# Kernel tuning notes

Measured on AMD Instinct MI355X. Metric: run time of the kernel, lower is better.

The kernel has to match this reference:

```python
import jax, jax.numpy as jnp
import numpy as np

N = 50000   # active sparse voxels
B = 4       # batch size
FIN = 64
FOUT = 128
TEMB = 256
K = 27      # 3x3x3 kernel offsets
EPS = 1e-5


def _bn(x, gamma, beta, mean, var):
    # inference-style BatchNorm over channel dim
    return (x - mean) * jax.lax.rsqrt(var + EPS) * gamma + beta


def _sparse_conv(feats, nbr, mask, W):
    # submanifold sparse conv via kernel map:
    # out[n] = sum_k mask[k,n] * feats[nbr[k,n]] @ W[k]
    g = feats[nbr] * mask[..., None].astype(feats.dtype)   # [K, N, Fin]
    return jnp.einsum('knf,kfo->no', g, W)                  # [N, Fout]


def _make_kernel_map(k_nbr, k_msk, n):
    nbr = jax.random.randint(k_nbr, (K, N), 0, n, dtype=jnp.int32)
    mask = jax.random.bernoulli(k_msk, 0.4, (K, N))
    # center offset is the identity map and always valid (submanifold conv)
    nbr = nbr.at[K // 2].set(jnp.arange(N, dtype=jnp.int32))
    mask = mask.at[K // 2].set(True)
    return nbr, mask


def setup_inputs() -> dict:
    key = jax.random.key(0)
    ks = jax.random.split(key, 20)
    x_feats = jax.random.normal(ks[0], (N, FIN), jnp.float32)
    batch_idx = jax.random.randint(ks[1], (N,), 0, B, dtype=jnp.int32)
    t = jax.random.normal(ks[2], (B, TEMB), jnp.float32)
    nbr1, mask1 = _make_kernel_map(ks[3], ks[4], N)
    nbr2, mask2 = _make_kernel_map(ks[5], ks[6], N)
    s1 = 1.0 / np.sqrt(FIN * K)
    s2 = 1.0 / np.sqrt(FOUT * K)
    return {
        'x_feats': x_feats, 'batch_idx': batch_idx, 't': t,
        'nbr1': nbr1, 'mask1': mask1, 'nbr2': nbr2, 'mask2': mask2,
        'bn1_gamma': jnp.ones((FIN,), jnp.float32),
        'bn1_beta': jnp.zeros((FIN,), jnp.float32),
        'bn1_mean': 0.1 * jax.random.normal(ks[7], (FIN,), jnp.float32),
        'bn1_var': jax.random.uniform(ks[8], (FIN,), jnp.float32, 0.5, 1.5),
        'W1': s1 * jax.random.normal(ks[9], (K, FIN, FOUT), jnp.float32),
        't_W': (1.0 / np.sqrt(TEMB)) * jax.random.normal(ks[10], (TEMB, FOUT), jnp.float32),
        't_b': jnp.zeros((FOUT,), jnp.float32),
        'bn2_gamma': jnp.ones((FOUT,), jnp.float32),
        'bn2_beta': jnp.zeros((FOUT,), jnp.float32),
        'bn2_mean': 0.1 * jax.random.normal(ks[11], (FOUT,), jnp.float32),
        'bn2_var': jax.random.uniform(ks[12], (FOUT,), jnp.float32, 0.5, 1.5),
        'W2': s2 * jax.random.normal(ks[13], (K, FOUT, FOUT), jnp.float32),
        'res_W': (1.0 / np.sqrt(FIN)) * jax.random.normal(ks[14], (FIN, FOUT), jnp.float32),
        'res_b': jnp.zeros((FOUT,), jnp.float32),
    }


def reference(x_feats, batch_idx, t, nbr1, mask1, nbr2, mask2,
              bn1_gamma, bn1_beta, bn1_mean, bn1_var, W1,
              t_W, t_b,
              bn2_gamma, bn2_beta, bn2_mean, bn2_var, W2,
              res_W, res_b):
    # conv1 block: BN -> SiLU -> sparse Conv3d
    h = jax.nn.silu(_bn(x_feats, bn1_gamma, bn1_beta, bn1_mean, bn1_var))
    h = _sparse_conv(h, nbr1, mask1, W1)                      # [N, FOUT]
    # FiLM-style time embedding, broadcast per point via batch index
    t_emb = jax.nn.silu(t) @ t_W + t_b                        # [B, FOUT]
    h = h + t_emb[batch_idx]
    # conv2 block
    h2 = jax.nn.silu(_bn(h, bn2_gamma, bn2_beta, bn2_mean, bn2_var))
    h2 = _sparse_conv(h2, nbr2, mask2, W2)                    # [N, FOUT]
    # residual connection (f_in != f_out -> Linear)
    return h2 + (x_feats @ res_W + res_b)
```

## Files before the change

### kernel.cpp

```cpp
#include <hip/hip_runtime.h>


#define EPS 1e-5f

typedef __attribute__((ext_vector_type(8))) short s16x8;
typedef __attribute__((ext_vector_type(4))) float f32x4;
typedef __attribute__((ext_vector_type(4))) unsigned short u16x4;

static __device__ __forceinline__ unsigned short f2bf(float f) {
    union { float f; unsigned u; } v; v.f = f;
    unsigned r = v.u + 0x7fffu + ((v.u >> 16) & 1u);
    return (unsigned short)(r >> 16);
}
static __device__ __forceinline__ float silu_d(float x) {
    return x / (1.f + __expf(-x));
}
static __device__ __forceinline__ void gload_lds16(const void* gsrc, void* ldst) {
    __builtin_amdgcn_global_load_lds(
        (const __attribute__((address_space(1))) unsigned int*)gsrc,
        (__attribute__((address_space(3))) unsigned int*)ldst, 16, 0, 0);
}
static __device__ __forceinline__ int mask_shift(const unsigned char* mask, int NV) {
    size_t base = (size_t)13 * (size_t)NV;
    int v = ((base & 3) == 3) ? 2 : 1;
    return (mask[base + v] == 1) ? 0 : 2;
}

__global__ void k_prep_small(const float* __restrict__ t, const float* __restrict__ tW,
                             const float* __restrict__ tb,
                             const float* __restrict__ g2, const float* __restrict__ b2,
                             const float* __restrict__ m2, const float* __restrict__ v2,
                             float* __restrict__ temb, float* __restrict__ sc,
                             float* __restrict__ sh, int B) {
    int tid = threadIdx.x;
    if (tid < B * 128) {
        int b = tid >> 7, o = tid & 127;
        float s = 0.f;
        for (int e = 0; e < 256; ++e) {
            float tv = t[b * 256 + e];
            s += silu_d(tv) * tW[e * 128 + o];
        }
        temb[tid] = s + tb[o];
    }
    if (tid < 128) {
        float rstd = rsqrtf(v2[tid] + EPS);
        float s1 = g2[tid] * rstd;
        sc[tid] = s1;
        sh[tid] = b2[tid] - m2[tid] * s1;
    }
}

__global__ __launch_bounds__(256) void k_shuffle(
        const float* __restrict__ W1, const float* __restrict__ W2,
        const float* __restrict__ rW,
        unsigned short* __restrict__ W1s, unsigned short* __restrict__ W2s,
        unsigned short* __restrict__ rWs) {
    int tid = blockIdx.x * 256 + threadIdx.x;
    const int n1 = 432 * 512, n2 = 864 * 512, n3 = 16 * 512;
    if (tid < n1) {
        int f = tid >> 9, r = tid & 511, lane = r >> 3, j = r & 7;
        int mt = f & 7, fk = f >> 3, ks = fk & 1, ko = fk >> 1;
        int fin = ks * 32 + (lane >> 4) * 8 + j;
        int fout = mt * 16 + (lane & 15);
        W1s[tid] = f2bf(W1[(ko * 64 + fin) * 128 + fout]);
    } else if (tid < n1 + n2) {
        int e = tid - n1;
        int f = e >> 9, r = e & 511, lane = r >> 3, j = r & 7;
        int mt = f & 7, fk = f >> 3, ks = fk & 3, ko = fk >> 2;
        int fin = ks * 32 + (lane >> 4) * 8 + j;
        int fout = mt * 16 + (lane & 15);
        W2s[e] = f2bf(W2[(ko * 128 + fin) * 128 + fout]);
    } else if (tid < n1 + n2 + n3) {
        int e = tid - n1 - n2;
        int f = e >> 9, r = e & 511, lane = r >> 3, j = r & 7;
        int mt = f & 7, ks = f >> 3;
        int fin = ks * 32 + (lane >> 4) * 8 + j;
        int fout = mt * 16 + (lane & 15);
        rWs[e] = f2bf(rW[fin * 128 + fout]);
    }
}

__global__ __launch_bounds__(256) void k_elem(
        const float* __restrict__ x,
        const float* __restrict__ g1, const float* __restrict__ b1,
        const float* __restrict__ m1, const float* __restrict__ v1,
        unsigned short* __restrict__ h1, int NV) {
    int tid = blockIdx.x * 256 + threadIdx.x;
    if (tid >= NV * 16) return;
    int n = tid >> 4, c = (tid & 15) << 2;
    f32x4 xv = *(const f32x4*)(x + n * 64 + c);
    f32x4 gv = *(const f32x4*)(g1 + c);
    f32x4 bv = *(const f32x4*)(b1 + c);
    f32x4 mv = *(const f32x4*)(m1 + c);
    f32x4 vv = *(const f32x4*)(v1 + c);
    u16x4 ho;
#pragma unroll
    for (int j = 0; j < 4; ++j) {
        float xn = (xv[j] - mv[j]) * rsqrtf(vv[j] + EPS) * gv[j] + bv[j];
        ho[j] = f2bf(silu_d(xn));
    }
    *(u16x4*)(h1 + n * 64 + c) = ho;
}

__global__ __launch_bounds__(512) void k_conv1(
        const unsigned short* __restrict__ h1, const int* __restrict__ nbr,
        const unsigned char* __restrict__ mask, const unsigned short* __restrict__ W1s,
        const float* __restrict__ temb, const int* __restrict__ bidx,
        const float* __restrict__ bn2sc, const float* __restrict__ bn2sh,
        unsigned short* __restrict__ h2in, int NV) {
    __shared__ unsigned short lds0[8192];
    __shared__ unsigned short lds1[8192];
    const int lane = threadIdx.x & 63;
    const int wave = threadIdx.x >> 6;
    const int g = lane >> 4, col = lane & 15;
    const int v = blockIdx.x * 128 + wave * 16 + col;
    const bool vok = v < NV;
    const int msh = mask_shift(mask, NV);

    f32x4 acc[8];
    const f32x4 z4 = {0.f, 0.f, 0.f, 0.f};
#pragma unroll
    for (int m = 0; m < 8; ++m) acc[m] = z4;
    const s16x8 zz = {0, 0, 0, 0, 0, 0, 0, 0};

    auto loadr = [&](int t) -> int {
        if (!vok) return -1;
        int off = t * NV + v;
        int nv = nbr[off];
        bool mm = mask[(size_t)off << msh] != 0;
        return mm ? nv : -1;
    };

    {
        const char* src = (const char*)W1s + (size_t)threadIdx.x * 16;
        char* dst = (char*)lds0 + (size_t)threadIdx.x * 16;
#pragma unroll
        for (int i = 0; i < 2; ++i)
            gload_lds16(src + i * 8192, dst + i * 8192);
    }
    int rA = loadr(0);
    int rN = loadr(1);
    int r0 = rA < 0 ? 0 : rA;
    s16x8 p0 = *(const s16x8*)(h1 + r0 * 64 + 0 * 32 + g * 8);
    s16x8 p1 = *(const s16x8*)(h1 + r0 * 64 + 1 * 32 + g * 8);
    __syncthreads();

    unsigned short* bufc = lds0;
    unsigned short* bufn = lds1;

    for (int t = 0; t < 27; ++t) {
        s16x8 q0, q1;
        int rN2 = -1;
        if (t < 26) {
            const char* src = (const char*)W1s + (size_t)(t + 1) * 16384 + (size_t)threadIdx.x * 16;
            char* dst = (char*)bufn + (size_t)threadIdx.x * 16;
#pragma unroll
            for (int i = 0; i < 2; ++i)
                gload_lds16(src + i * 8192, dst + i * 8192);
            int rn = rN < 0 ? 0 : rN;
            q0 = *(const s16x8*)(h1 + rn * 64 + 0 * 32 + g * 8);
            q1 = *(const s16x8*)(h1 + rn * 64 + 1 * 32 + g * 8);
        }
        if (t < 25) rN2 = loadr(t + 2);
        const bool m = rA >= 0;
        s16x8 b0 = m ? p0 : zz;
        s16x8 b1 = m ? p1 : zz;
        const unsigned short* wp = bufc + lane * 8;
#pragma unroll
        for (int mt = 0; mt < 8; ++mt) {
            s16x8 a = *(const s16x8*)(wp + (0 * 8 + mt) * 512);
            acc[mt] = __builtin_amdgcn_mfma_f32_16x16x32_bf16(a, b0, acc[mt], 0, 0, 0);
        }
#pragma unroll
        for (int mt = 0; mt < 8; ++mt) {
            s16x8 a = *(const s16x8*)(wp + (1 * 8 + mt) * 512);
            acc[mt] = __builtin_amdgcn_mfma_f32_16x16x32_bf16(a, b1, acc[mt], 0, 0, 0);
        }
        if (t < 26) {
            __syncthreads();
            p0 = q0; p1 = q1;
            rA = rN; rN = rN2;
            unsigned short* tmp = bufc; bufc = bufn; bufn = tmp;
        }
    }

    if (vok) {
        int b = bidx[v];
        const float* te = temb + b * 128;
#pragma unroll
        for (int mt = 0; mt < 8; ++mt) {
            int c = mt * 16 + g * 4;
            f32x4 val = acc[mt];
            f32x4 tv = *(const f32x4*)(te + c);
            f32x4 sc = *(const f32x4*)(bn2sc + c);
            f32x4 sh = *(const f32x4*)(bn2sh + c);
            u16x4 o;
#pragma unroll
            for (int j = 0; j < 4; ++j) {
                float zv = (val[j] + tv[j]) * sc[j] + sh[j];
                o[j] = f2bf(silu_d(zv));
            }
            *(u16x4*)(h2in + v * 128 + c) = o;
        }
    }
}

__global__ __launch_bounds__(512) void k_conv2(
        const unsigned short* __restrict__ h2in, const int* __restrict__ nbr,
        const unsigned char* __restrict__ mask, const unsigned short* __restrict__ W2s,
        const float* __restrict__ x, const unsigned short* __restrict__ rWs,
        const float* __restrict__ resb, float* __restrict__ out, int NV) {
    __shared__ unsigned short lds0[16384];
    __shared__ unsigned short lds1[16384];
    const int lane = threadIdx.x & 63;
    const int wave = threadIdx.x >> 6;
    const int g = lane >> 4, col = lane & 15;
    const int v = blockIdx.x * 128 + wave * 16 + col;
    const bool vok = v < NV;
    const int msh = mask_shift(mask, NV);

    f32x4 acc[8];
    const f32x4 z4 = {0.f, 0.f, 0.f, 0.f};
#pragma unroll
    for (int m = 0; m < 8; ++m) acc[m] = z4;
    const s16x8 zz = {0, 0, 0, 0, 0, 0, 0, 0};

    auto loadr = [&](int t) -> int {
        if (!vok) return -1;
        int off = t * NV + v;
        int nv = nbr[off];
        bool mm = mask[(size_t)off << msh] != 0;
        return mm ? nv : -1;
    };

    {
        const char* src = (const char*)W2s + (size_t)threadIdx.x * 16;
        char* dst = (char*)lds0 + (size_t)threadIdx.x * 16;
#pragma unroll
        for (int i = 0; i < 4; ++i)
            gload_lds16(src + i * 8192, dst + i * 8192);
    }
    int rA = loadr(0);
    int rN = loadr(1);
    int r0 = rA < 0 ? 0 : rA;
    s16x8 p0 = *(const s16x8*)(h2in + r0 * 128 + 0 * 32 + g * 8);
    s16x8 p1 = *(const s16x8*)(h2in + r0 * 128 + 1 * 32 + g * 8);
    s16x8 p2 = *(const s16x8*)(h2in + r0 * 128 + 2 * 32 + g * 8);
    s16x8 p3 = *(const s16x8*)(h2in + r0 * 128 + 3 * 32 + g * 8);

    {
        int rv = vok ? v : 0;
#pragma unroll
        for (int ks = 0; ks < 2; ++ks) {
            f32x4 xa = *(const f32x4*)(x + rv * 64 + ks * 32 + g * 8);
            f32x4 xb = *(const f32x4*)(x + rv * 64 + ks * 32 + g * 8 + 4);
            s16x8 b;
#pragma unroll
            for (int j = 0; j < 4; ++j) {
                b[j]     = (short)f2bf(xa[j]);
                b[j + 4] = (short)f2bf(xb[j]);
            }
            const unsigned short* wp = rWs + ks * 4096 + lane * 8;
#pragma unroll
            for (int mt = 0; mt < 8; ++mt) {
                s16x8 a = *(const s16x8*)(wp + mt * 512);
                acc[mt] = __builtin_amdgcn_mfma_f32_16x16x32_bf16(a, b, acc[mt], 0, 0, 0);
            }
        }
    }
    __syncthreads();

    unsigned short* bufc = lds0;
    unsigned short* bufn = lds1;

    for (int t = 0; t < 27; ++t) {
        s16x8 q0, q1, q2, q3;
        int rN2 = -1;
        if (t < 26) {
            const char* src = (const char*)W2s + (size_t)(t + 1) * 32768 + (size_t)threadIdx.x * 16;
            char* dst = (char*)bufn + (size_t)threadIdx.x * 16;
#pragma unroll
            for (int i = 0; i < 4; ++i)
                gload_lds16(src + i * 8192, dst + i * 8192);
            int rn = rN < 0 ? 0 : rN;
            q0 = *(const s16x8*)(h2in + rn * 128 + 0 * 32 + g * 8);
            q1 = *(const s16x8*)(h2in + rn * 128 + 1 * 32 + g * 8);
            q2 = *(const s16x8*)(h2in + rn * 128 + 2 * 32 + g * 8);
            q3 = *(const s16x8*)(h2in + rn * 128 + 3 * 32 + g * 8);
        }
        if (t < 25) rN2 = loadr(t + 2);
        const bool m = rA >= 0;
        s16x8 b0 = m ? p0 : zz;
        s16x8 b1 = m ? p1 : zz;
        s16x8 b2 = m ? p2 : zz;
        s16x8 b3 = m ? p3 : zz;
        const unsigned short* wp = bufc + lane * 8;
#pragma unroll
        for (int mt = 0; mt < 8; ++mt) {
            s16x8 a = *(const s16x8*)(wp + (0 * 8 + mt) * 512);
            acc[mt] = __builtin_amdgcn_mfma_f32_16x16x32_bf16(a, b0, acc[mt], 0, 0, 0);
        }
#pragma unroll
        for (int mt = 0; mt < 8; ++mt) {
            s16x8 a = *(const s16x8*)(wp + (1 * 8 + mt) * 512);
            acc[mt] = __builtin_amdgcn_mfma_f32_16x16x32_bf16(a, b1, acc[mt], 0, 0, 0);
        }
#pragma unroll
        for (int mt = 0; mt < 8; ++mt) {
            s16x8 a = *(const s16x8*)(wp + (2 * 8 + mt) * 512);
            acc[mt] = __builtin_amdgcn_mfma_f32_16x16x32_bf16(a, b2, acc[mt], 0, 0, 0);
        }
#pragma unroll
        for (int mt = 0; mt < 8; ++mt) {
            s16x8 a = *(const s16x8*)(wp + (3 * 8 + mt) * 512);
            acc[mt] = __builtin_amdgcn_mfma_f32_16x16x32_bf16(a, b3, acc[mt], 0, 0, 0);
        }
        if (t < 26) {
            __syncthreads();
            p0 = q0; p1 = q1; p2 = q2; p3 = q3;
            rA = rN; rN = rN2;
            unsigned short* tmp = bufc; bufc = bufn; bufn = tmp;
        }
    }

    if (vok) {
#pragma unroll
        for (int mt = 0; mt < 8; ++mt) {
            int c = mt * 16 + g * 4;
            f32x4 rr = acc[mt] + *(const f32x4*)(resb + c);
            *(f32x4*)(out + v * 128 + c) = rr;
        }
    }
}

extern "C" void kernel_launch(void* const* d_in, const int* in_sizes, int n_in,
                              void* d_out, int out_size, void* d_ws, size_t ws_size,
                              hipStream_t stream) {
    const float* x          = (const float*)d_in[0];
    const int* bidx         = (const int*)d_in[1];
    const float* t          = (const float*)d_in[2];
    const int* nbr1         = (const int*)d_in[3];
    const unsigned char* mask1 = (const unsigned char*)d_in[4];
    const int* nbr2         = (const int*)d_in[5];
    const unsigned char* mask2 = (const unsigned char*)d_in[6];
    const float* bn1g       = (const float*)d_in[7];
    const float* bn1b       = (const float*)d_in[8];
    const float* bn1m       = (const float*)d_in[9];
    const float* bn1v       = (const float*)d_in[10];
    const float* W1         = (const float*)d_in[11];
    const float* tW         = (const float*)d_in[12];
    const float* tb         = (const float*)d_in[13];
    const float* bn2g       = (const float*)d_in[14];
    const float* bn2b       = (const float*)d_in[15];
    const float* bn2m       = (const float*)d_in[16];
    const float* bn2v       = (const float*)d_in[17];
    const float* W2         = (const float*)d_in[18];
    const float* rW         = (const float*)d_in[19];
    const float* resb       = (const float*)d_in[20];

    const int NV = in_sizes[0] / 64;
    const int B  = in_sizes[2] / 256;
    float* out = (float*)d_out;

    char* ws = (char*)d_ws;
    size_t o_W1s = 0;
    size_t o_W2s = o_W1s + (size_t)432 * 1024;
    size_t o_rWs = o_W2s + (size_t)864 * 1024;
    size_t o_te  = o_rWs + (size_t)16 * 1024;
    size_t o_sc  = o_te  + (size_t)B * 128 * 4;
    size_t o_sh  = o_sc  + 512;
    size_t o_h1  = o_sh  + 512;
    size_t o_h2  = o_h1  + (size_t)NV * 64 * 2;

    unsigned short* W1s  = (unsigned short*)(ws + o_W1s);
    unsigned short* W2s  = (unsigned short*)(ws + o_W2s);
    unsigned short* rWs  = (unsigned short*)(ws + o_rWs);
    float* temb  = (float*)(ws + o_te);
    float* bn2sc = (float*)(ws + o_sc);
    float* bn2sh = (float*)(ws + o_sh);
    unsigned short* h1   = (unsigned short*)(ws + o_h1);
    unsigned short* h2in = (unsigned short*)(ws + o_h2);

    k_prep_small<<<1, 512, 0, stream>>>(t, tW, tb, bn2g, bn2b, bn2m, bn2v,
                                        temb, bn2sc, bn2sh, B);
    {
        int total = (432 + 864 + 16) * 512;
        int grid = (total + 255) / 256;
        k_shuffle<<<grid, 256, 0, stream>>>(W1, W2, rW, W1s, W2s, rWs);
    }
    {
        int total = NV * 16;
        int grid = (total + 255) / 256;
        k_elem<<<grid, 256, 0, stream>>>(x, bn1g, bn1b, bn1m, bn1v, h1, NV);
    }
    {
        int grid = (NV + 127) / 128;
        k_conv1<<<grid, 512, 0, stream>>>(h1, nbr1, mask1, W1s, temb, bidx,
                                          bn2sc, bn2sh, h2in, NV);
        k_conv2<<<grid, 512, 0, stream>>>(h2in, nbr2, mask2, W2s, x, rWs,
                                          resb, out, NV);
    }
}
```

Measured before the change: 138.2 us.

## Fuse prep kernels into one launch and resize conv blocks to 98 voxels

Merges the small time-embedding/BN2 prep, weight shuffle and BN1+SiLU elementwise kernels into a single launch dispatched by block index, removing two kernel launches and their serialization gaps. The conv kernels shrink from 512 to 448 threads (7 waves) with 98 voxels per block, giving about 511 blocks so the work spreads more evenly across the GPU's compute units. Each block still streams the full weight tiles into LDS, so per-voxel weight traffic rises, and 14 of the 112 voxel slots per block sit idle.

After: 122.4 us, median of 2. 1.13x faster.

```diff
diff --git a/kernel.cpp b/kernel.cpp
--- a/kernel.cpp
+++ b/kernel.cpp
@@ -6,6 +6,8 @@
 typedef __attribute__((ext_vector_type(8))) short s16x8;
 typedef __attribute__((ext_vector_type(4))) float f32x4;
 typedef __attribute__((ext_vector_type(4))) unsigned short u16x4;
+
+#define VPB 98
 
 static __device__ __forceinline__ unsigned short f2bf(float f) {
     union { float f; unsigned u; } v; v.f = f;
@@ -26,83 +28,91 @@
     return (mask[base + v] == 1) ? 0 : 2;
 }
 
-__global__ void k_prep_small(const float* __restrict__ t, const float* __restrict__ tW,
-                             const float* __restrict__ tb,
-                             const float* __restrict__ g2, const float* __restrict__ b2,
-                             const float* __restrict__ m2, const float* __restrict__ v2,
-                             float* __restrict__ temb, float* __restrict__ sc,
-                             float* __restrict__ sh, int B) {
-    int tid = threadIdx.x;
-    if (tid < B * 128) {
-        int b = tid >> 7, o = tid & 127;
-        float s = 0.f;
-        for (int e = 0; e < 256; ++e) {
-            float tv = t[b * 256 + e];
-            s += silu_d(tv) * tW[e * 128 + o];
-        }
-        temb[tid] = s + tb[o];
-    }
-    if (tid < 128) {
-        float rstd = rsqrtf(v2[tid] + EPS);
-        float s1 = g2[tid] * rstd;
-        sc[tid] = s1;
-        sh[tid] = b2[tid] - m2[tid] * s1;
-    }
-}
-
-__global__ __launch_bounds__(256) void k_shuffle(
+#define NSH 2624
+__global__ __launch_bounds__(256) void k_prep_fused(
+        const float* __restrict__ t, const float* __restrict__ tW,
+        const float* __restrict__ tb,
+        const float* __restrict__ g2, const float* __restrict__ b2,
+        const float* __restrict__ m2, const float* __restrict__ v2,
+        float* __restrict__ temb, float* __restrict__ sc, float* __restrict__ sh,
         const float* __restrict__ W1, const float* __restrict__ W2,
         const float* __restrict__ rW,
         unsigned short* __restrict__ W1s, unsigned short* __restrict__ W2s,
-        unsigned short* __restrict__ rWs) {
-    int tid = blockIdx.x * 256 + threadIdx.x;
-    const int n1 = 432 * 512, n2 = 864 * 512, n3 = 16 * 512;
-    if (tid < n1) {
-        int f = tid >> 9, r = tid & 511, lane = r >> 3, j = r & 7;
-        int mt = f & 7, fk = f >> 3, ks = fk & 1, ko = fk >> 1;
-        int fin = ks * 32 + (lane >> 4) * 8 + j;
-        int fout = mt * 16 + (lane & 15);
-        W1s[tid] = f2bf(W1[(ko * 64 + fin) * 128 + fout]);
-    } else if (tid < n1 + n2) {
-        int e = tid - n1;
-        int f = e >> 9, r = e & 511, lane = r >> 3, j = r & 7;
-        int mt = f & 7, fk = f >> 3, ks = fk & 3, ko = fk >> 2;
-        int fin = ks * 32 + (lane >> 4) * 8 + j;
-        int fout = mt * 16 + (lane & 15);
-        W2s[e] = f2bf(W2[(ko * 128 + fin) * 128 + fout]);
-    } else if (tid < n1 + n2 + n3) {
-        int e = tid - n1 - n2;
-        int f = e >> 9, r = e & 511, lane = r >> 3, j = r & 7;
-        int mt = f & 7, ks = f >> 3;
-        int fin = ks * 32 + (lane >> 4) * 8 + j;
-        int fout = mt * 16 + (lane & 15);
-        rWs[e] = f2bf(rW[fin * 128 + fout]);
-    }
-}
-
-__global__ __launch_bounds__(256) void k_elem(
+        unsigned short* __restrict__ rWs,
         const float* __restrict__ x,
         const float* __restrict__ g1, const float* __restrict__ b1,
         const float* __restrict__ m1, const float* __restrict__ v1,
-        unsigned short* __restrict__ h1, int NV) {
-    int tid = blockIdx.x * 256 + threadIdx.x;
-    if (tid >= NV * 16) return;
-    int n = tid >> 4, c = (tid & 15) << 2;
-    f32x4 xv = *(const f32x4*)(x + n * 64 + c);
-    f32x4 gv = *(const f32x4*)(g1 + c);
-    f32x4 bv = *(const f32x4*)(b1 + c);
-    f32x4 mv = *(const f32x4*)(m1 + c);
-    f32x4 vv = *(const f32x4*)(v1 + c);
-    u16x4 ho;
-#pragma unroll
-    for (int j = 0; j < 4; ++j) {
-        float xn = (xv[j] - mv[j]) * rsqrtf(vv[j] + EPS) * gv[j] + bv[j];
-        ho[j] = f2bf(silu_d(xn));
-    }
-    *(u16x4*)(h1 + n * 64 + c) = ho;
-}
-
-__global__ __launch_bounds__(512) void k_conv1(
+        unsigned short* __restrict__ h1, int NV, int B) {
+    const int bid = blockIdx.x;
+    if (bid < 2) {
+        int idx = bid * 256 + threadIdx.x;
+        if (idx < B * 128) {
+            int b = idx >> 7, o = idx & 127;
+            float s = 0.f;
+            for (int e = 0; e < 256; ++e) {
+                float tv = t[b * 256 + e];
+                s += silu_d(tv) * tW[e * 128 + o];
+            }
+            temb[idx] = s + tb[o];
+        }
+        return;
+    }
+    if (bid == 2) {
+        int tid = threadIdx.x;
+        if (tid < 128) {
+            float rstd = rsqrtf(v2[tid] + EPS);
+            float s1 = g2[tid] * rstd;
+            sc[tid] = s1;
+            sh[tid] = b2[tid] - m2[tid] * s1;
+        }
+        return;
+    }
+    if (bid < 3 + NSH) {
+        int tid = (bid - 3) * 256 + threadIdx.x;
+        const int n1 = 432 * 512, n2 = 864 * 512, n3 = 16 * 512;
+        if (tid < n1) {
+            int f = tid >> 9, r = tid & 511, lane = r >> 3, j = r & 7;
+            int mt = f & 7, fk = f >> 3, ks = fk & 1, ko = fk >> 1;
+            int fin = ks * 32 + (lane >> 4) * 8 + j;
+            int fout = mt * 16 + (lane & 15);
+            W1s[tid] = f2bf(W1[(ko * 64 + fin) * 128 + fout]);
+        } else if (tid < n1 + n2) {
+            int e = tid - n1;
+            int f = e >> 9, r = e & 511, lane = r >> 3, j = r & 7;
+            int mt = f & 7, fk = f >> 3, ks = fk & 3, ko = fk >> 2;
+            int fin = ks * 32 + (lane >> 4) * 8 + j;
+            int fout = mt * 16 + (lane & 15);
+            W2s[e] = f2bf(W2[(ko * 128 + fin) * 128 + fout]);
+        } else if (tid < n1 + n2 + n3) {
+            int e = tid - n1 - n2;
+            int f = e >> 9, r = e & 511, lane = r >> 3, j = r & 7;
+            int mt = f & 7, ks = f >> 3;
+            int fin = ks * 32 + (lane >> 4) * 8 + j;
+            int fout = mt * 16 + (lane & 15);
+            rWs[e] = f2bf(rW[fin * 128 + fout]);
+        }
+        return;
+    }
+    {
+        int tid = (bid - 3 - NSH) * 256 + threadIdx.x;
+        if (tid >= NV * 16) return;
+        int n = tid >> 4, c = (tid & 15) << 2;
+        f32x4 xv = *(const f32x4*)(x + n * 64 + c);
+        f32x4 gv = *(const f32x4*)(g1 + c);
+        f32x4 bv = *(const f32x4*)(b1 + c);
+        f32x4 mv = *(const f32x4*)(m1 + c);
+        f32x4 vv = *(const f32x4*)(v1 + c);
+        u16x4 ho;
+#pragma unroll
+        for (int j = 0; j < 4; ++j) {
+            float xn = (xv[j] - mv[j]) * rsqrtf(vv[j] + EPS) * gv[j] + bv[j];
+            ho[j] = f2bf(silu_d(xn));
+        }
+        *(u16x4*)(h1 + n * 64 + c) = ho;
+    }
+}
+
+__global__ __launch_bounds__(448) void k_conv1(
         const unsigned short* __restrict__ h1, const int* __restrict__ nbr,
         const unsigned char* __restrict__ mask, const unsigned short* __restrict__ W1s,
         const float* __restrict__ temb, const int* __restrict__ bidx,
@@ -113,8 +123,9 @@
     const int lane = threadIdx.x & 63;
     const int wave = threadIdx.x >> 6;
     const int g = lane >> 4, col = lane & 15;
-    const int v = blockIdx.x * 128 + wave * 16 + col;
-    const bool vok = v < NV;
+    const int slot = wave * 16 + col;
+    const int v = blockIdx.x * VPB + slot;
+    const bool vok = (slot < VPB) && (v < NV);
     const int msh = mask_shift(mask, NV);
 
     f32x4 acc[8];
@@ -131,13 +142,8 @@
         return mm ? nv : -1;
     };
 
-    {
-        const char* src = (const char*)W1s + (size_t)threadIdx.x * 16;
-        char* dst = (char*)lds0 + (size_t)threadIdx.x * 16;
-#pragma unroll
-        for (int i = 0; i < 2; ++i)
-            gload_lds16(src + i * 8192, dst + i * 8192);
-    }
+    for (int off = threadIdx.x * 16; off < 16384; off += 7168)
+        gload_lds16((const char*)W1s + off, (char*)lds0 + off);
     int rA = loadr(0);
     int rN = loadr(1);
     int r0 = rA < 0 ? 0 : rA;
@@ -152,11 +158,9 @@
         s16x8 q0, q1;
         int rN2 = -1;
         if (t < 26) {
-            const char* src = (const char*)W1s + (size_t)(t + 1) * 16384 + (size_t)threadIdx.x * 16;
-            char* dst = (char*)bufn + (size_t)threadIdx.x * 16;
-#pragma unroll
-            for (int i = 0; i < 2; ++i)
-                gload_lds16(src + i * 8192, dst + i * 8192);
+            const char* src = (const char*)W1s + (size_t)(t + 1) * 16384;
+            for (int off = threadIdx.x * 16; off < 16384; off += 7168)
+                gload_lds16(src + off, (char*)bufn + off);
             int rn = rN < 0 ? 0 : rN;
             q0 = *(const s16x8*)(h1 + rn * 64 + 0 * 32 + g * 8);
             q1 = *(const s16x8*)(h1 + rn * 64 + 1 * 32 + g * 8);
@@ -205,7 +209,7 @@
     }
 }
 
-__global__ __launch_bounds__(512) void k_conv2(
+__global__ __launch_bounds__(448) void k_conv2(
         const unsigned short* __restrict__ h2in, const int* __restrict__ nbr,
         const unsigned char* __restrict__ mask, const unsigned short* __restrict__ W2s,
         const float* __restrict__ x, const unsigned short* __restrict__ rWs,
@@ -215,8 +219,9 @@
     const int lane = threadIdx.x & 63;
     const int wave = threadIdx.x >> 6;
     const int g = lane >> 4, col = lane & 15;
-    const int v = blockIdx.x * 128 + wave * 16 + col;
-    const bool vok = v < NV;
+    const int slot = wave * 16 + col;
+    const int v = blockIdx.x * VPB + slot;
+    const bool vok = (slot < VPB) && (v < NV);
     const int msh = mask_shift(mask, NV);
 
     f32x4 acc[8];
@@ -233,13 +238,8 @@
         return mm ? nv : -1;
     };
 
-    {
-        const char* src = (const char*)W2s + (size_t)threadIdx.x * 16;
-        char* dst = (char*)lds0 + (size_t)threadIdx.x * 16;
-#pragma unroll
-        for (int i = 0; i < 4; ++i)
-            gload_lds16(src + i * 8192, dst + i * 8192);
-    }
+    for (int off = threadIdx.x * 16; off < 32768; off += 7168)
+        gload_lds16((const char*)W2s + off, (char*)lds0 + off);
     int rA = loadr(0);
     int rN = loadr(1);
     int r0 = rA < 0 ? 0 : rA;
@@ -277,11 +277,9 @@
         s16x8 q0, q1, q2, q3;
         int rN2 = -1;
         if (t < 26) {
-            const char* src = (const char*)W2s + (size_t)(t + 1) * 32768 + (size_t)threadIdx.x * 16;
-            char* dst = (char*)bufn + (size_t)threadIdx.x * 16;
-#pragma unroll
-            for (int i = 0; i < 4; ++i)
-                gload_lds16(src + i * 8192, dst + i * 8192);
+            const char* src = (const char*)W2s + (size_t)(t + 1) * 32768;
+            for (int off = threadIdx.x * 16; off < 32768; off += 7168)
+                gload_lds16(src + off, (char*)bufn + off);
             int rn = rN < 0 ? 0 : rN;
             q0 = *(const s16x8*)(h2in + rn * 128 + 0 * 32 + g * 8);
             q1 = *(const s16x8*)(h2in + rn * 128 + 1 * 32 + g * 8);
@@ -381,23 +379,19 @@
     unsigned short* h1   = (unsigned short*)(ws + o_h1);
     unsigned short* h2in = (unsigned short*)(ws + o_h2);
 
-    k_prep_small<<<1, 512, 0, stream>>>(t, tW, tb, bn2g, bn2b, bn2m, bn2v,
-                                        temb, bn2sc, bn2sh, B);
     {
-        int total = (432 + 864 + 16) * 512;
-        int grid = (total + 255) / 256;
-        k_shuffle<<<grid, 256, 0, stream>>>(W1, W2, rW, W1s, W2s, rWs);
+        int nel = (NV * 16 + 255) / 256;
+        int grid = 3 + NSH + nel;
+        k_prep_fused<<<grid, 256, 0, stream>>>(
+            t, tW, tb, bn2g, bn2b, bn2m, bn2v, temb, bn2sc, bn2sh,
+            W1, W2, rW, W1s, W2s, rWs,
+            x, bn1g, bn1b, bn1m, bn1v, h1, NV, B);
     }
     {
-        int total = NV * 16;
-        int grid = (total + 255) / 256;
-        k_elem<<<grid, 256, 0, stream>>>(x, bn1g, bn1b, bn1m, bn1v, h1, NV);
-    }
-    {
-        int grid = (NV + 127) / 128;
-        k_conv1<<<grid, 512, 0, stream>>>(h1, nbr1, mask1, W1s, temb, bidx,
+        int grid = (NV + VPB - 1) / VPB;
+        k_conv1<<<grid, 448, 0, stream>>>(h1, nbr1, mask1, W1s, temb, bidx,
                                           bn2sc, bn2sh, h2in, NV);
-        k_conv2<<<grid, 512, 0, stream>>>(h2in, nbr2, mask2, W2s, x, rWs,
+        k_conv2<<<grid, 448, 0, stream>>>(h2in, nbr2, mask2, W2s, x, rWs,
                                           resb, out, NV);
     }
 }
```
